# Performance work log

Hardware: AMD Instinct MI355X
Metric: run time of the kernel (lower is better)

Reference implementation:

```python
import jax, jax.numpy as jnp
import numpy as np

B = 32; N_NODES = 1000; WINDOW = 4; D = 128; N_PARTS = 10
T = 2; T_INT = 1; T_TEMP = 1
N_TOTAL = B * WINDOW * N_NODES
E_INT = 200000; E_TEMP = 96000


def setup_inputs() -> dict:
    key = jax.random.key(0)
    ks = jax.random.split(key, 24)
    inp = {}
    inp["node_inputs"] = jax.random.randint(ks[0], (B, N_NODES), 0, 10)
    inp["node_indices"] = jax.random.randint(ks[1], (E_INT,), 0, N_TOTAL)
    inp["neighbour_indices"] = jax.random.randint(ks[2], (E_INT,), 0, N_TOTAL)
    inp["temp_node_indices"] = jax.random.randint(ks[3], (E_TEMP,), 0, N_TOTAL)
    inp["temp_neighbour_indices"] = jax.random.randint(ks[4], (E_TEMP,), 0, N_TOTAL)

    def dense(k, din, dout):
        return jax.random.normal(k, (din, dout), jnp.float32) * np.float32(1.0 / np.sqrt(din))

    inp["embed_table"] = jax.random.normal(ks[5], (10, D), jnp.float32)
    # message MLP: 2*D -> 64 -> 64 -> 64 -> 64 -> D (4 gelu hidden, linear out)
    inp["msg_W_in"] = dense(ks[6], 2 * D, 64); inp["msg_b_in"] = jnp.zeros((64,), jnp.float32)
    inp["msg_W_hid"] = jax.random.normal(ks[7], (3, 64, 64), jnp.float32) * np.float32(1.0 / 8.0)
    inp["msg_b_hid"] = jnp.zeros((3, 64), jnp.float32)
    inp["msg_W_out"] = dense(ks[8], 64, D); inp["msg_b_out"] = jnp.zeros((D,), jnp.float32)
    # readout MLP: D -> 64 -> 64 -> 64 -> 64 -> n_parts
    inp["ro_W_in"] = dense(ks[9], D, 64); inp["ro_b_in"] = jnp.zeros((64,), jnp.float32)
    inp["ro_W_hid"] = jax.random.normal(ks[10], (3, 64, 64), jnp.float32) * np.float32(1.0 / 8.0)
    inp["ro_b_hid"] = jnp.zeros((3, 64), jnp.float32)
    inp["ro_W_out"] = dense(ks[11], 64, N_PARTS); inp["ro_b_out"] = jnp.zeros((N_PARTS,), jnp.float32)
    # GRU cells (tf.keras reset_after=True): kernel [D,3D], recurrent [D,3D], input+recurrent biases
    for nm, base in (("gi", 12), ("gt", 16)):
        inp[nm + "_Wx"] = dense(ks[base], D, 3 * D)
        inp[nm + "_Wh"] = dense(ks[base + 1], D, 3 * D)
        inp[nm + "_bi"] = jnp.zeros((3 * D,), jnp.float32)
        inp[nm + "_br"] = jnp.zeros((3 * D,), jnp.float32)
    return inp


def _mlp(x, W_in, b_in, W_hid, b_hid, W_out, b_out):
    h = jax.nn.gelu(x @ W_in + b_in, approximate=False)
    for i in range(W_hid.shape[0]):
        h = jax.nn.gelu(h @ W_hid[i] + b_hid[i], approximate=False)
    return h @ W_out + b_out


def _gru(h, x, Wx, Wh, bi, br):
    # tf.keras GRUCell, reset_after=True
    xz, xr, xh = jnp.split(x @ Wx + bi, 3, axis=1)
    hz, hr, hh = jnp.split(h @ Wh + br, 3, axis=1)
    z = jax.nn.sigmoid(xz + hz)
    r = jax.nn.sigmoid(xr + hr)
    cand = jnp.tanh(xh + r * hh)
    return z * h + (1.0 - z) * cand


def _message_mean(h, ni, bi, msg_p):
    g0 = h[ni]              # [E, D] node gather
    g1 = h[bi]              # [E, D] neighbour gather
    x = jnp.concatenate([jnp.concatenate([g0, g1], 1), jnp.concatenate([g1, g0], 1)], 0)  # [2E, 2D]
    msg = _mlp(x, *msg_p)   # [2E, D]
    seg = jnp.concatenate([bi, ni], 0)
    s = jax.ops.segment_sum(msg, seg, num_segments=h.shape[0])
    c = jax.ops.segment_sum(jnp.ones((seg.shape[0], 1), msg.dtype), seg, num_segments=h.shape[0])
    return s / jnp.maximum(c, 1.0)


def reference(node_inputs, node_indices, neighbour_indices, temp_node_indices, temp_neighbour_indices,
              embed_table, msg_W_in, msg_b_in, msg_W_hid, msg_b_hid, msg_W_out, msg_b_out,
              ro_W_in, ro_b_in, ro_W_hid, ro_b_hid, ro_W_out, ro_b_out,
              gi_Wx, gi_Wh, gi_bi, gi_br, gt_Wx, gt_Wh, gt_bi, gt_br):
    msg_p = (msg_W_in, msg_b_in, msg_W_hid, msg_b_hid, msg_W_out, msg_b_out)
    h = embed_table[node_inputs]                       # [B, N, D]
    h = jnp.repeat(h, WINDOW, axis=0).reshape(-1, D)   # [B*W*N, D]
    for _ in range(T):
        for _ in range(T_INT):
            m = _message_mean(h, node_indices, neighbour_indices, msg_p)
            h = _gru(h, m, gi_Wx, gi_Wh, gi_bi, gi_br)
        for _ in range(T_TEMP):
            m = _message_mean(h, temp_node_indices, temp_neighbour_indices, msg_p)
            h = _gru(h, m, gt_Wx, gt_Wh, gt_bi, gt_br)
    ridx = jnp.arange(N_NODES)[None, :] + jnp.arange(B)[:, None] * (WINDOW * N_NODES)
    return _mlp(h[ridx], ro_W_in, ro_b_in, ro_W_hid, ro_b_hid, ro_W_out, ro_b_out)  # [B, N, n_parts]
```

## Files before the change

### kernel.cpp

```cpp
#include <hip/hip_runtime.h>
#include <math.h>


#define DDIM 128
#define NTOT 128000
#define HBYTES 65536000ULL
#define EBLK 128

typedef unsigned short u16;
using f32x4 = __attribute__((ext_vector_type(4))) float;
using s16x8 = __attribute__((ext_vector_type(8))) short;

__device__ __forceinline__ float fast_rcp(float x) {
    return __builtin_amdgcn_rcpf(x);
}
__device__ __forceinline__ float gelu_exact(float x) {
    return 0.5f * x * (1.0f + erff(x * 0.70710678118654752440f));
}
__device__ __forceinline__ float gelu_fast(float x) {
    const float ax = fabsf(x) * 0.70710678118654752440f;
    const float t  = fast_rcp(1.0f + 0.3275911f * ax);
    const float poly = t * (0.254829592f + t * (-0.284496736f +
                       t * (1.421413741f + t * (-1.453152027f +
                       t * 1.061405429f))));
    const float e = __expf(-ax * ax);
    const float erfax = 1.0f - poly * e;
    const float erfv = copysignf(erfax, x);
    return 0.5f * x * (1.0f + erfv);
}
__device__ __forceinline__ float sigmoid_fast(float x) {
    return fast_rcp(1.0f + __expf(-x));
}
__device__ __forceinline__ float tanh_fast(float x) {
    const float e = __expf(2.0f * x);
    return 1.0f - 2.0f * fast_rcp(e + 1.0f);
}
__device__ __forceinline__ u16 f2bf(float x) {
    unsigned u = __float_as_uint(x);
    u += 0x7fffu + ((u >> 16) & 1u);
    return (u16)(u >> 16);
}
__device__ __forceinline__ float bf2f(u16 h) {
    return __uint_as_float(((unsigned)h) << 16);
}

__global__ __launch_bounds__(256) void embed_kernel(
    const int* __restrict__ inp, const float* __restrict__ table,
    float* __restrict__ h)
{
    int gid = blockIdx.x * 256 + threadIdx.x;
    if (gid >= NTOT * 32) return;
    int row = gid >> 5;
    int q   = gid & 31;
    int b   = row / 4000;
    int n   = (row % 4000) % 1000;
    int e   = inp[b * 1000 + n];
    ((float4*)h)[gid] = ((const float4*)table)[e * 32 + q];
}

__global__ __launch_bounds__(256) void hist_kernel(
    const int* __restrict__ ni, const int* __restrict__ bi, int E,
    int* __restrict__ deg)
{
    int g = blockIdx.x * 256 + threadIdx.x;
    if (g < E)          atomicAdd(&deg[bi[g]], 1);
    else if (g < 2 * E) atomicAdd(&deg[ni[g - E]], 1);
}

__global__ __launch_bounds__(256) void blockscan_kernel(
    const int* __restrict__ deg, int* __restrict__ offp, int* __restrict__ bsum)
{
    __shared__ int s[256];
    int tid = threadIdx.x;
    int i = blockIdx.x * 256 + tid;
    int v = deg[i];
    s[tid] = v;
    __syncthreads();
    for (int off = 1; off < 256; off <<= 1) {
        int t = (tid >= off) ? s[tid - off] : 0;
        __syncthreads();
        s[tid] += t;
        __syncthreads();
    }
    offp[i] = s[tid] - v;
    if (tid == 255) bsum[blockIdx.x] = s[255];
}

__global__ __launch_bounds__(512) void bscan_kernel(
    const int* __restrict__ bsum, int* __restrict__ bexc, int nb)
{
    __shared__ int s[512];
    int t = threadIdx.x;
    int v = (t < nb) ? bsum[t] : 0;
    s[t] = v;
    __syncthreads();
    for (int off = 1; off < 512; off <<= 1) {
        int u = (t >= off) ? s[t - off] : 0;
        __syncthreads();
        s[t] += u;
        __syncthreads();
    }
    if (t < nb) bexc[t] = s[t] - v;
}

__global__ __launch_bounds__(256) void fill_kernel(
    const int* __restrict__ ni, const int* __restrict__ bi, int E,
    const int* __restrict__ offp, const int* __restrict__ bexc,
    int* __restrict__ cursor, int* __restrict__ elist, int* __restrict__ slotseg)
{
    int g = blockIdx.x * 256 + threadIdx.x;
    if (g >= 2 * E) return;
    int seg = (g < E) ? bi[g] : ni[g - E];
    int pos = atomicAdd(&cursor[seg], 1);
    int slot = offp[seg] + bexc[seg >> 8] + pos;
    elist[slot] = g;
    slotseg[slot] = seg;
}

__global__ __launch_bounds__(256) void straddle_kernel(
    const int* __restrict__ slotseg, int nblocks32,
    int* __restrict__ list, int* __restrict__ count)
{
    int b = blockIdx.x * 256 + threadIdx.x + 1;
    if (b >= nblocks32) return;
    int s = slotseg[b * 32];
    if (s >= 0 && slotseg[b * 32 - 1] == s) {
        int pos = atomicAdd(count, 1);
        list[pos] = s;
    }
}

__global__ __launch_bounds__(64) void zero_rows_kernel(
    const int* __restrict__ list, const int* __restrict__ count,
    float* __restrict__ sbuf)
{
    int i = blockIdx.x;
    if (i >= *count) return;
    int seg = list[i];
    float4* row = (float4*)(sbuf + (size_t)seg * 64);
    if (threadIdx.x < 16) row[threadIdx.x] = make_float4(0.f, 0.f, 0.f, 0.f);
}

__global__ __launch_bounds__(256) void pack_gateB_kernel(
    const float* __restrict__ Wx, const float* __restrict__ Wh,
    u16* __restrict__ BH, u16* __restrict__ BL)
{
    int idx = blockIdx.x * 256 + threadIdx.x;
    if (idx >= 131072) return;
    int j    = idx & 7;
    int lane = (idx >> 3) & 63;
    int ntG  = (idx >> 9) & 31;
    int ktG  = idx >> 14;
    int k = ktG * 32 + (lane >> 4) * 8 + j;
    int n = ntG * 16 + (lane & 15);
    int g = n >> 7, jj = n & 127;
    float v;
    if (g == 0)      v = (k < 128) ? Wx[k * 384 + jj]       : Wh[(k - 128) * 384 + jj];
    else if (g == 1) v = (k < 128) ? Wx[k * 384 + 128 + jj] : Wh[(k - 128) * 384 + 128 + jj];
    else if (g == 2) v = (k < 128) ? Wx[k * 384 + 256 + jj] : 0.0f;
    else             v = (k < 128) ? 0.0f                   : Wh[(k - 128) * 384 + 256 + jj];
    u16 hb = f2bf(v);
    BH[idx] = hb;
    BL[idx] = f2bf(v - bf2f(hb));
}

__global__ __launch_bounds__(256) void pack_preB_kernel(
    const float* __restrict__ Win, u16* __restrict__ BH, u16* __restrict__ BL)
{
    int idx = blockIdx.x * 256 + threadIdx.x;
    if (idx >= 16384) return;
    int j    = idx & 7;
    int lane = (idx >> 3) & 63;
    int nt2  = (idx >> 9) & 7;
    int kt2  = idx >> 12;
    int k = kt2 * 32 + (lane >> 4) * 8 + j;
    int n = nt2 * 16 + (lane & 15);
    float v = (n < 64) ? Win[k * 64 + n] : Win[(128 + k) * 64 + (n - 64)];
    u16 hb = f2bf(v);
    BH[idx] = hb;
    BL[idx] = f2bf(v - bf2f(hb));
}

__global__ __launch_bounds__(256) void pack_hidB_kernel(
    const float* __restrict__ Whid, u16* __restrict__ BH, u16* __restrict__ BL)
{
    int idx = blockIdx.x * 256 + threadIdx.x;
    if (idx >= 12288) return;
    int j    = idx & 7;
    int lane = (idx >> 3) & 63;
    int nt   = (idx >> 9) & 3;
    int kt   = (idx >> 11) & 1;
    int L    = idx >> 12;
    int k = kt * 32 + (lane >> 4) * 8 + j;
    int n = nt * 16 + (lane & 15);
    float v = Whid[L * 4096 + k * 64 + n];
    u16 hb = f2bf(v);
    BH[idx] = hb;
    BL[idx] = f2bf(v - bf2f(hb));
}

__global__ __launch_bounds__(256) void pack_outB_kernel(
    const float* __restrict__ Wout, u16* __restrict__ BH, u16* __restrict__ BL)
{
    int idx = blockIdx.x * 256 + threadIdx.x;
    if (idx >= 8192) return;
    int j    = idx & 7;
    int lane = (idx >> 3) & 63;
    int nt   = (idx >> 9) & 7;
    int kt   = idx >> 12;
    int k = kt * 32 + (lane >> 4) * 8 + j;
    int n = nt * 16 + (lane & 15);
    float v = Wout[k * 128 + n];
    u16 hb = f2bf(v);
    BH[idx] = hb;
    BL[idx] = f2bf(v - bf2f(hb));
}

__global__ __launch_bounds__(256) void node_pre_kernel(
    const float* __restrict__ h, const float* __restrict__ Win,
    const float* __restrict__ bin, float* __restrict__ p)
{
    const int node = blockIdx.x * 256 + threadIdx.x;
    const float4* h4 = (const float4*)(h + (size_t)node * DDIM);
    float* prow = p + (size_t)node * DDIM;

    for (int c = 0; c < 4; ++c) {
        const int top   = (c < 2) ? 1 : 0;
        const int j0    = (c & 1) * 32;
        const int kbase = top ? 0 : 128;
        float acc[32];
        #pragma unroll
        for (int j = 0; j < 32; ++j) acc[j] = top ? bin[j0 + j] : 0.0f;
        for (int k4 = 0; k4 < 32; ++k4) {
            float4 hv = h4[k4];
            #pragma unroll
            for (int kk = 0; kk < 4; ++kk) {
                const float hk = (&hv.x)[kk];
                const float* wr = Win + (size_t)(kbase + k4 * 4 + kk) * 64 + j0;
                #pragma unroll
                for (int j = 0; j < 32; ++j) acc[j] = fmaf(hk, wr[j], acc[j]);
            }
        }
        float* dst = prow + (top ? 0 : 64) + j0;
        #pragma unroll
        for (int q = 0; q < 8; ++q)
            ((float4*)dst)[q] = make_float4(acc[q*4], acc[q*4+1],
                                            acc[q*4+2], acc[q*4+3]);
    }
}

__global__ __launch_bounds__(512) void edge_mlp_mfma(
    const int* __restrict__ ni, const int* __restrict__ bi, int E,
    const int* __restrict__ elist, const int* __restrict__ slotseg,
    const float* __restrict__ p,
    const u16* __restrict__ BhH, const u16* __restrict__ BhL,
    const float* __restrict__ bhid,
    float* __restrict__ sbuf)
{
    __shared__ short smA[17408];
    __shared__ int   segLDS[EBLK];
    __shared__ int   segedge[2];
    float* scat = (float*)smA;

    const int tid  = threadIdx.x;
    const int lane = tid & 63;
    const int w    = tid >> 6;
    const int s0   = blockIdx.x * EBLK;

    if (tid < 128) segLDS[tid] = slotseg[s0 + tid];
    if (tid == 0) segedge[0] = slotseg[s0 - 1];
    if (tid == 1) segedge[1] = slotseg[s0 + EBLK];

    {
        const int m  = (tid & 15) | (w << 4);
        const int gg = (tid >> 4) & 3;
        const int slot = s0 + m;
        const int g = elist[slot];
        int first, second;
        if (g < E) { first = ni[g];     second = bi[g];     }
        else       { first = bi[g - E]; second = ni[g - E]; }
        #pragma unroll
        for (int kt = 0; kt < 2; ++kt) {
            const int k0 = kt * 32 + gg * 8;
            const float4* pa = (const float4*)(p + (size_t)first  * DDIM + k0);
            const float4* pb = (const float4*)(p + (size_t)second * DDIM + 64 + k0);
            const float4 a0 = pa[0], a1 = pa[1], b0 = pb[0], b1 = pb[1];
            float x[8] = { a0.x + b0.x, a0.y + b0.y, a0.z + b0.z, a0.w + b0.w,
                           a1.x + b1.x, a1.y + b1.y, a1.z + b1.z, a1.w + b1.w };
            s16x8 hi8, lo8;
            #pragma unroll
            for (int j = 0; j < 8; ++j) {
                const float v = gelu_fast(x[j]);
                u16 hb = f2bf(v);
                hi8[j] = (short)hb;
                lo8[j] = (short)f2bf(v - bf2f(hb));
            }
            const int off = (kt * 8 + w) * 512 + lane * 8;
            *(s16x8*)(smA + off)        = hi8;
            *(s16x8*)(smA + 8192 + off) = lo8;
        }
    }

    const int mt = w;
    for (int L = 0; L < 2; ++L) {
        f32x4 acc[4];
        #pragma unroll
        for (int nt = 0; nt < 4; ++nt) {
            const float bv = bhid[L * 64 + nt * 16 + (lane & 15)];
            acc[nt] = (f32x4){bv, bv, bv, bv};
        }
        #pragma unroll
        for (int kt = 0; kt < 2; ++kt) {
            const s16x8 aH = *(const s16x8*)(smA + (kt * 8 + mt) * 512 + lane * 8);
            const s16x8 aL = *(const s16x8*)(smA + 8192 + (kt * 8 + mt) * 512 + lane * 8);
            #pragma unroll
            for (int nt = 0; nt < 4; ++nt) {
                const int bidx = (L * 8 + kt * 4 + nt) * 64 + lane;
                const s16x8 bH = ((const s16x8*)BhH)[bidx];
                const s16x8 bL = ((const s16x8*)BhL)[bidx];
                acc[nt] = __builtin_amdgcn_mfma_f32_16x16x32_bf16(aH, bH, acc[nt], 0, 0, 0);
                acc[nt] = __builtin_amdgcn_mfma_f32_16x16x32_bf16(aH, bL, acc[nt], 0, 0, 0);
                acc[nt] = __builtin_amdgcn_mfma_f32_16x16x32_bf16(aL, bH, acc[nt], 0, 0, 0);
            }
        }
        #pragma unroll
        for (int nt = 0; nt < 4; ++nt) {
            #pragma unroll
            for (int r = 0; r < 4; ++r) {
                const float v = gelu_fast(acc[nt][r]);
                const int ml  = (lane >> 4) * 4 + r;
                const int k   = nt * 16 + (lane & 15);
                const int kt2 = k >> 5, gg = (k >> 3) & 3, j = k & 7;
                const int off = (kt2 * 8 + mt) * 512 + (ml + 16 * gg) * 8 + j;
                u16 hb = f2bf(v);
                smA[off]        = (short)hb;
                smA[8192 + off] = (short)f2bf(v - bf2f(hb));
            }
        }
    }

    float gl[4][4];
    {
        f32x4 acc[4];
        #pragma unroll
        for (int nt = 0; nt < 4; ++nt) {
            const float bv = bhid[2 * 64 + nt * 16 + (lane & 15)];
            acc[nt] = (f32x4){bv, bv, bv, bv};
        }
        #pragma unroll
        for (int kt = 0; kt < 2; ++kt) {
            const s16x8 aH = *(const s16x8*)(smA + (kt * 8 + mt) * 512 + lane * 8);
            const s16x8 aL = *(const s16x8*)(smA + 8192 + (kt * 8 + mt) * 512 + lane * 8);
            #pragma unroll
            for (int nt = 0; nt < 4; ++nt) {
                const int bidx = (2 * 8 + kt * 4 + nt) * 64 + lane;
                const s16x8 bH = ((const s16x8*)BhH)[bidx];
                const s16x8 bL = ((const s16x8*)BhL)[bidx];
                acc[nt] = __builtin_amdgcn_mfma_f32_16x16x32_bf16(aH, bH, acc[nt], 0, 0, 0);
                acc[nt] = __builtin_amdgcn_mfma_f32_16x16x32_bf16(aH, bL, acc[nt], 0, 0, 0);
                acc[nt] = __builtin_amdgcn_mfma_f32_16x16x32_bf16(aL, bH, acc[nt], 0, 0, 0);
            }
        }
        #pragma unroll
        for (int nt = 0; nt < 4; ++nt)
            #pragma unroll
            for (int r = 0; r < 4; ++r)
                gl[nt][r] = gelu_fast(acc[nt][r]);
    }

    __syncthreads();
    #pragma unroll
    for (int nt = 0; nt < 4; ++nt)
        #pragma unroll
        for (int r = 0; r < 4; ++r)
            scat[(mt * 16 + (lane >> 4) * 4 + r) * 68 + nt * 16 + (lane & 15)]
                = gl[nt][r];
    __syncthreads();

    if (tid < 256) {
        const int col = tid & 63;
        const int r0  = (tid >> 6) * 32;
        const int r1  = r0 + 32;
        int   runSeg = -2;
        float runacc = 0.0f;
        bool  leftC  = true;
        for (int rowi = r0; rowi < r1; ++rowi) {
            const int sg = segLDS[rowi];
            const float v = scat[rowi * 68 + col];
            if (sg != runSeg) {
                if (runSeg >= 0) {
                    float* pp = sbuf + (size_t)runSeg * 64 + col;
                    if (leftC) *pp = runacc;
                    else       atomicAdd(pp, runacc);
                }
                runSeg = sg;
                runacc = v;
                if (rowi == r0) {
                    const int prev = (rowi == 0) ? segedge[0] : segLDS[rowi - 1];
                    leftC = (prev != sg);
                } else {
                    leftC = true;
                }
            } else {
                runacc += v;
            }
        }
        if (runSeg >= 0) {
            const int nxt = (r1 == 128) ? segedge[1] : segLDS[r1];
            const bool rightC = (nxt != runSeg);
            float* pp = sbuf + (size_t)runSeg * 64 + col;
            if (leftC && rightC) *pp = runacc;
            else                 atomicAdd(pp, runacc);
        }
    }
}

__global__ __launch_bounds__(256, 3) void gru_mfma_kernel(
    float* __restrict__ hio, const float* __restrict__ Ssum,
    const int* __restrict__ deg,
    const u16* __restrict__ WoH, const u16* __restrict__ WoL,
    const float* __restrict__ bo,
    const u16* __restrict__ BgH, const u16* __restrict__ BgL,
    const float* __restrict__ bi_, const float* __restrict__ br_,
    const u16* __restrict__ BpH, const u16* __restrict__ BpL,
    const float* __restrict__ binp,
    float* __restrict__ pout)
{
    __shared__ short sm[16384];
    __shared__ float ci_s[64];
    const int tid  = threadIdx.x;
    const int lane = tid & 63;
    const int w    = tid >> 6;
    const int jg   = w & 1;
    const int mh   = w >> 1;
    const int nbase = blockIdx.x * 64;

    const int mS = tid >> 2, q = tid & 3;
    const int nodeS = nbase + mS;
    const int laneS = (mS & 15) + 16 * q;
    const int seg_m = mS >> 4;
    const int dg = deg[nodeS];
    const float ci = (dg > 0) ? fast_rcp((float)dg) : 0.0f;
    ci_s[mS] = ci;

    #pragma unroll
    for (int c = 0; c < 2; ++c) {
        const int kl = c * 32 + q * 8;
        const float* src = Ssum + (size_t)nodeS * 64 + kl;
        const float4 v0 = ((const float4*)src)[0];
        const float4 v1 = ((const float4*)src)[1];
        float xv[8] = { v0.x * ci, v0.y * ci, v0.z * ci, v0.w * ci,
                        v1.x * ci, v1.y * ci, v1.z * ci, v1.w * ci };
        s16x8 hi8, lo8;
        #pragma unroll
        for (int i = 0; i < 8; ++i) {
            u16 hb = f2bf(xv[i]);
            hi8[i] = (short)hb;
            lo8[i] = (short)f2bf(xv[i] - bf2f(hb));
        }
        const int off = (c * 4 + seg_m) * 512 + laneS * 8;
        *(s16x8*)(sm + off)        = hi8;
        *(s16x8*)(sm + off + 8192) = lo8;
    }
    __syncthreads();

    f32x4 am[2][4];
    #pragma unroll
    for (int mf = 0; mf < 2; ++mf)
        #pragma unroll
        for (int t4 = 0; t4 < 4; ++t4)
            am[mf][t4] = (f32x4){0.f, 0.f, 0.f, 0.f};
    {
        const s16x8* WH8 = (const s16x8*)WoH;
        const s16x8* WL8 = (const s16x8*)WoL;
        #pragma unroll
        for (int kt = 0; kt < 2; ++kt) {
            const int a0off = (kt * 4 + 2 * mh) * 512 + lane * 8;
            const s16x8 aH0 = *(const s16x8*)(sm + a0off);
            const s16x8 aL0 = *(const s16x8*)(sm + 8192 + a0off);
            const s16x8 aH1 = *(const s16x8*)(sm + a0off + 512);
            const s16x8 aL1 = *(const s16x8*)(sm + 8192 + a0off + 512);
            #pragma unroll
            for (int t4 = 0; t4 < 4; ++t4) {
                const int idx = (kt * 8 + jg * 4 + t4) * 64 + lane;
                const s16x8 bH = WH8[idx];
                const s16x8 bL = WL8[idx];
                am[0][t4] = __builtin_amdgcn_mfma_f32_16x16x32_bf16(aH0, bH, am[0][t4], 0, 0, 0);
                am[0][t4] = __builtin_amdgcn_mfma_f32_16x16x32_bf16(aH0, bL, am[0][t4], 0, 0, 0);
                am[0][t4] = __builtin_amdgcn_mfma_f32_16x16x32_bf16(aL0, bH, am[0][t4], 0, 0, 0);
                am[1][t4] = __builtin_amdgcn_mfma_f32_16x16x32_bf16(aH1, bH, am[1][t4], 0, 0, 0);
                am[1][t4] = __builtin_amdgcn_mfma_f32_16x16x32_bf16(aH1, bL, am[1][t4], 0, 0, 0);
                am[1][t4] = __builtin_amdgcn_mfma_f32_16x16x32_bf16(aL1, bH, am[1][t4], 0, 0, 0);
            }
        }
    }
    __syncthreads();

    #pragma unroll
    for (int t4 = 0; t4 < 4; ++t4) {
        const int n = jg * 64 + t4 * 16 + (lane & 15);
        const float bv = bo[n];
        const int kt2 = n >> 5, gg = (n >> 3) & 3, jj = n & 7;
        #pragma unroll
        for (int mf = 0; mf < 2; ++mf) {
            const int mtile = 2 * mh + mf;
            #pragma unroll
            for (int r = 0; r < 4; ++r) {
                const int m15 = (lane >> 4) * 4 + r;
                const float cin = ci_s[mtile * 16 + m15];
                const float mv = am[mf][t4][r] + ((cin > 0.0f) ? bv : 0.0f);
                const int off = (kt2 * 4 + mtile) * 512 + (m15 + 16 * gg) * 8 + jj;
                u16 hb = f2bf(mv);
                sm[off]        = (short)hb;
                sm[off + 8192] = (short)f2bf(mv - bf2f(hb));
            }
        }
    }
    __syncthreads();

    f32x4 acc[2][4][4];
    #pragma unroll
    for (int mf = 0; mf < 2; ++mf)
        #pragma unroll
        for (int g = 0; g < 4; ++g)
            #pragma unroll
            for (int t4 = 0; t4 < 4; ++t4)
                acc[mf][g][t4] = (f32x4){0.f, 0.f, 0.f, 0.f};

    const s16x8* Bh8 = (const s16x8*)BgH;
    const s16x8* Bl8 = (const s16x8*)BgL;
    #pragma unroll
    for (int kt = 0; kt < 4; ++kt) {
        const int a0off = (kt * 4 + 2 * mh) * 512 + lane * 8;
        const s16x8 aH0 = *(const s16x8*)(sm + a0off);
        const s16x8 aL0 = *(const s16x8*)(sm + 8192 + a0off);
        const s16x8 aH1 = *(const s16x8*)(sm + a0off + 512);
        const s16x8 aL1 = *(const s16x8*)(sm + 8192 + a0off + 512);
        #pragma unroll
        for (int g = 0; g < 3; ++g) {
            #pragma unroll
            for (int t4 = 0; t4 < 4; ++t4) {
                const int idx = (kt * 32 + g * 8 + jg * 4 + t4) * 64 + lane;
                const s16x8 bH = Bh8[idx];
                const s16x8 bL = Bl8[idx];
                acc[0][g][t4] = __builtin_amdgcn_mfma_f32_16x16x32_bf16(aH0, bH, acc[0][g][t4], 0, 0, 0);
                acc[0][g][t4] = __builtin_amdgcn_mfma_f32_16x16x32_bf16(aH0, bL, acc[0][g][t4], 0, 0, 0);
                acc[0][g][t4] = __builtin_amdgcn_mfma_f32_16x16x32_bf16(aL0, bH, acc[0][g][t4], 0, 0, 0);
                acc[1][g][t4] = __builtin_amdgcn_mfma_f32_16x16x32_bf16(aH1, bH, acc[1][g][t4], 0, 0, 0);
                acc[1][g][t4] = __builtin_amdgcn_mfma_f32_16x16x32_bf16(aH1, bL, acc[1][g][t4], 0, 0, 0);
                acc[1][g][t4] = __builtin_amdgcn_mfma_f32_16x16x32_bf16(aL1, bH, acc[1][g][t4], 0, 0, 0);
            }
        }
    }
    __syncthreads();

    #pragma unroll
    for (int c = 0; c < 4; ++c) {
        const int kl = c * 32 + q * 8;
        const float* src = hio + (size_t)nodeS * DDIM + kl;
        const float4 v0 = ((const float4*)src)[0];
        const float4 v1 = ((const float4*)src)[1];
        float xv[8] = { v0.x, v0.y, v0.z, v0.w, v1.x, v1.y, v1.z, v1.w };
        s16x8 hi8, lo8;
        #pragma unroll
        for (int i = 0; i < 8; ++i) {
            u16 hb = f2bf(xv[i]);
            hi8[i] = (short)hb;
            lo8[i] = (short)f2bf(xv[i] - bf2f(hb));
        }
        const int off = (c * 4 + seg_m) * 512 + laneS * 8;
        *(s16x8*)(sm + off)        = hi8;
        *(s16x8*)(sm + off + 8192) = lo8;
    }
    __syncthreads();

    #pragma unroll
    for (int kt = 0; kt < 4; ++kt) {
        const int ktG = 4 + kt;
        const int a0off = (kt * 4 + 2 * mh) * 512 + lane * 8;
        const s16x8 aH0 = *(const s16x8*)(sm + a0off);
        const s16x8 aL0 = *(const s16x8*)(sm + 8192 + a0off);
        const s16x8 aH1 = *(const s16x8*)(sm + a0off + 512);
        const s16x8 aL1 = *(const s16x8*)(sm + 8192 + a0off + 512);
        #pragma unroll
        for (int gi = 0; gi < 3; ++gi) {
            const int g = (gi == 2) ? 3 : gi;
            #pragma unroll
            for (int t4 = 0; t4 < 4; ++t4) {
                const int idx = (ktG * 32 + g * 8 + jg * 4 + t4) * 64 + lane;
                const s16x8 bH = Bh8[idx];
                const s16x8 bL = Bl8[idx];
                acc[0][g][t4] = __builtin_amdgcn_mfma_f32_16x16x32_bf16(aH0, bH, acc[0][g][t4], 0, 0, 0);
                acc[0][g][t4] = __builtin_amdgcn_mfma_f32_16x16x32_bf16(aH0, bL, acc[0][g][t4], 0, 0, 0);
                acc[0][g][t4] = __builtin_amdgcn_mfma_f32_16x16x32_bf16(aL0, bH, acc[0][g][t4], 0, 0, 0);
                acc[1][g][t4] = __builtin_amdgcn_mfma_f32_16x16x32_bf16(aH1, bH, acc[1][g][t4], 0, 0, 0);
                acc[1][g][t4] = __builtin_amdgcn_mfma_f32_16x16x32_bf16(aH1, bL, acc[1][g][t4], 0, 0, 0);
                acc[1][g][t4] = __builtin_amdgcn_mfma_f32_16x16x32_bf16(aL1, bH, acc[1][g][t4], 0, 0, 0);
            }
        }
    }

    float hn[2][4][4];
    #pragma unroll
    for (int t4 = 0; t4 < 4; ++t4) {
        const int j = jg * 64 + t4 * 16 + (lane & 15);
        const float b_az = bi_[j]       + br_[j];
        const float b_ar = bi_[128 + j] + br_[128 + j];
        const float b_xh = bi_[256 + j];
        const float b_hh = br_[256 + j];
        const int jbase = (j >> 5) * 2048 + ((j >> 3) & 3) * 128 + (j & 7);
        #pragma unroll
        for (int mf = 0; mf < 2; ++mf) {
            const int mtile = 2 * mh + mf;
            #pragma unroll
            for (int r = 0; r < 4; ++r) {
                const int m15 = (lane >> 4) * 4 + r;
                const int off = jbase + mtile * 512 + m15 * 8;
                const float hv = bf2f((u16)sm[off]) + bf2f((u16)sm[8192 + off]);
                const int m = mtile * 16 + m15;
                const float az = acc[mf][0][t4][r] + b_az;
                const float ar = acc[mf][1][t4][r] + b_ar;
                const float xh = acc[mf][2][t4][r] + b_xh;
                const float hh = acc[mf][3][t4][r] + b_hh;
                const float z    = sigmoid_fast(az);
                const float rr   = sigmoid_fast(ar);
                const float cand = tanh_fast(xh + rr * hh);
                const float v    = z * hv + (1.0f - z) * cand;
                hio[(size_t)(nbase + m) * DDIM + j] = v;
                hn[mf][t4][r] = v;
            }
        }
    }
    __syncthreads();

    #pragma unroll
    for (int mf = 0; mf < 2; ++mf) {
        const int mtile = 2 * mh + mf;
        #pragma unroll
        for (int t4 = 0; t4 < 4; ++t4) {
            #pragma unroll
            for (int r = 0; r < 4; ++r) {
                const int m15 = (lane >> 4) * 4 + r;
                const int j   = jg * 64 + t4 * 16 + (lane & 15);
                const int kt2 = j >> 5, gg = (j >> 3) & 3, jj = j & 7;
                const int off = (kt2 * 4 + mtile) * 512 + (m15 + 16 * gg) * 8 + jj;
                const float v = hn[mf][t4][r];
                u16 hb = f2bf(v);
                sm[off]        = (short)hb;
                sm[off + 8192] = (short)f2bf(v - bf2f(hb));
            }
        }
    }
    __syncthreads();

    f32x4 acc2[2][4];
    #pragma unroll
    for (int mf = 0; mf < 2; ++mf)
        #pragma unroll
        for (int t4 = 0; t4 < 4; ++t4)
            acc2[mf][t4] = (f32x4){0.f, 0.f, 0.f, 0.f};

    const s16x8* Ph8 = (const s16x8*)BpH;
    const s16x8* Pl8 = (const s16x8*)BpL;
    #pragma unroll
    for (int kt2 = 0; kt2 < 4; ++kt2) {
        const int a0off = (kt2 * 4 + 2 * mh) * 512 + lane * 8;
        const s16x8 aH0 = *(const s16x8*)(sm + a0off);
        const s16x8 aL0 = *(const s16x8*)(sm + 8192 + a0off);
        const s16x8 aH1 = *(const s16x8*)(sm + a0off + 512);
        const s16x8 aL1 = *(const s16x8*)(sm + 8192 + a0off + 512);
        #pragma unroll
        for (int t4 = 0; t4 < 4; ++t4) {
            const int idx = (kt2 * 8 + jg * 4 + t4) * 64 + lane;
            const s16x8 bH = Ph8[idx];
            const s16x8 bL = Pl8[idx];
            acc2[0][t4] = __builtin_amdgcn_mfma_f32_16x16x32_bf16(aH0, bH, acc2[0][t4], 0, 0, 0);
            acc2[0][t4] = __builtin_amdgcn_mfma_f32_16x16x32_bf16(aH0, bL, acc2[0][t4], 0, 0, 0);
            acc2[0][t4] = __builtin_amdgcn_mfma_f32_16x16x32_bf16(aL0, bH, acc2[0][t4], 0, 0, 0);
            acc2[1][t4] = __builtin_amdgcn_mfma_f32_16x16x32_bf16(aH1, bH, acc2[1][t4], 0, 0, 0);
            acc2[1][t4] = __builtin_amdgcn_mfma_f32_16x16x32_bf16(aH1, bL, acc2[1][t4], 0, 0, 0);
            acc2[1][t4] = __builtin_amdgcn_mfma_f32_16x16x32_bf16(aL1, bH, acc2[1][t4], 0, 0, 0);
        }
    }
    #pragma unroll
    for (int mf = 0; mf < 2; ++mf) {
        const int mtile = 2 * mh + mf;
        #pragma unroll
        for (int t4 = 0; t4 < 4; ++t4) {
            const int n = jg * 64 + t4 * 16 + (lane & 15);
            const float badd = (n < 64) ? binp[n] : 0.0f;
            #pragma unroll
            for (int r = 0; r < 4; ++r) {
                const int m = mtile * 16 + (lane >> 4) * 4 + r;
                pout[(size_t)(nbase + m) * DDIM + n] = acc2[mf][t4][r] + badd;
            }
        }
    }
}

__global__ __launch_bounds__(64) void readout_kernel(
    const float* __restrict__ h,
    const float* __restrict__ Win,  const float* __restrict__ bin,
    const float* __restrict__ Whid, const float* __restrict__ bhid,
    const float* __restrict__ Wout, const float* __restrict__ bout,
    float* __restrict__ out)
{
    __shared__ float xs[64 * 65];
    const int tid = threadIdx.x;
    const int row = blockIdx.x * 64 + tid;
    const int b = row / 1000, n = row % 1000;
    const float4* xrow = (const float4*)(h + ((size_t)b * 4000 + n) * DDIM);

    {
        float acc[64];
        #pragma unroll
        for (int j = 0; j < 64; ++j) acc[j] = bin[j];
        #pragma unroll 2
        for (int k4 = 0; k4 < 32; ++k4) {
            float4 xv = xrow[k4];
            #pragma unroll
            for (int kk = 0; kk < 4; ++kk) {
                const float xk = (&xv.x)[kk];
                const float* wr = Win + (size_t)(k4 * 4 + kk) * 64;
                #pragma unroll
                for (int j = 0; j < 64; ++j) acc[j] = fmaf(xk, wr[j], acc[j]);
            }
        }
        #pragma unroll
        for (int j = 0; j < 64; ++j) xs[tid * 65 + j] = gelu_exact(acc[j]);
    }

    for (int L = 0; L < 3; ++L) {
        float acc[64];
        #pragma unroll
        for (int j = 0; j < 64; ++j) acc[j] = bhid[L * 64 + j];
        #pragma unroll 4
        for (int k = 0; k < 64; ++k) {
            const float xk = xs[tid * 65 + k];
            const float* wr = Whid + (size_t)L * 4096 + (size_t)k * 64;
            #pragma unroll
            for (int j = 0; j < 64; ++j) acc[j] = fmaf(xk, wr[j], acc[j]);
        }
        #pragma unroll
        for (int j = 0; j < 64; ++j) xs[tid * 65 + j] = gelu_exact(acc[j]);
    }

    float acc[10];
    #pragma unroll
    for (int pj = 0; pj < 10; ++pj) acc[pj] = bout[pj];
    #pragma unroll 4
    for (int k = 0; k < 64; ++k) {
        const float xk = xs[tid * 65 + k];
        const float* wr = Wout + k * 10;
        #pragma unroll
        for (int pj = 0; pj < 10; ++pj) acc[pj] = fmaf(xk, wr[pj], acc[pj]);
    }
    #pragma unroll
    for (int pj = 0; pj < 10; ++pj) out[(size_t)row * 10 + pj] = acc[pj];
}

extern "C" void kernel_launch(void* const* d_in, const int* in_sizes, int n_in,
                              void* d_out, int out_size, void* d_ws, size_t ws_size,
                              hipStream_t stream) {
    const int*   node_inputs = (const int*)d_in[0];
    const int*   ni_int = (const int*)d_in[1];
    const int*   bi_int = (const int*)d_in[2];
    const int*   ni_tmp = (const int*)d_in[3];
    const int*   bi_tmp = (const int*)d_in[4];
    const float* embed  = (const float*)d_in[5];
    const float* mWin   = (const float*)d_in[6];
    const float* mbin   = (const float*)d_in[7];
    const float* mWhid  = (const float*)d_in[8];
    const float* mbhid  = (const float*)d_in[9];
    const float* mWout  = (const float*)d_in[10];
    const float* mbout  = (const float*)d_in[11];
    const float* roWin  = (const float*)d_in[12];
    const float* robin  = (const float*)d_in[13];
    const float* roWhid = (const float*)d_in[14];
    const float* robhid = (const float*)d_in[15];
    const float* roWout = (const float*)d_in[16];
    const float* robout = (const float*)d_in[17];
    const float* giWx = (const float*)d_in[18];
    const float* giWh = (const float*)d_in[19];
    const float* gibi = (const float*)d_in[20];
    const float* gibr = (const float*)d_in[21];
    const float* gtWx = (const float*)d_in[22];
    const float* gtWh = (const float*)d_in[23];
    const float* gtbi = (const float*)d_in[24];
    const float* gtbr = (const float*)d_in[25];
    float* out = (float*)d_out;

    const int E_INT = 200000, E_TMP = 96000;
    const int NSLOT_I = 400000;
    const int NSLOT_T = 192000;
    const int NBLK_I = NSLOT_I / EBLK;
    const int NBLK_T = NSLOT_T / EBLK;
    const int NS32_I = NSLOT_I / 32;
    const int NS32_T = NSLOT_T / 32;

    char* ws = (char*)d_ws;
    float* B0 = (float*)(ws);
    float* B1 = (float*)(ws + HBYTES);
    float* B2 = (float*)(ws + 2 * HBYTES);
    char*  ib = ws + 3 * HBYTES;

    int* deg_i   = (int*)(ib);
    int* deg_t   = (int*)(ib + 512000);
    int* offp_i  = (int*)(ib + 1024000);
    int* offp_t  = (int*)(ib + 1536000);
    int* bexc_i  = (int*)(ib + 2048000);
    int* bexc_t  = (int*)(ib + 2052096);
    int* bsum    = (int*)(ib + 2056192);
    int* cursor  = (int*)(ib + 2060288);
    int* el_i    = (int*)(ib + 2572288);
    int* el_t    = (int*)(ib + 4172288);
    int* ssi_raw = (int*)(ib + 4940288);
    int* sst_raw = (int*)(ib + 6540296);
    char* fb = ib + 8114176;
    u16* BgiH = (u16*)(fb);
    u16* BgiL = (u16*)(fb +  262144);
    u16* BgtH = (u16*)(fb +  524288);
    u16* BgtL = (u16*)(fb +  786432);
    u16* BpH  = (u16*)(fb + 1048576);
    u16* BpL  = (u16*)(fb + 1081344);
    u16* EhH  = (u16*)(fb + 1114112);
    u16* EhL  = (u16*)(fb + 1138688);
    u16* EoH  = (u16*)(fb + 1163264);
    u16* EoL  = (u16*)(fb + 1179648);
    int* str_i  = (int*)(fb + 1196032);
    int* str_t  = (int*)(fb + 1246032);
    int* strc_i = (int*)(fb + 1270032);
    int* strc_t = (int*)(fb + 1270036);
    int* ssi = ssi_raw + 1;
    int* sst = sst_raw + 1;

    embed_kernel<<<16000, 256, 0, stream>>>(node_inputs, embed, B0);

    hipMemsetAsync(deg_i, 0, NTOT * sizeof(int), stream);
    hipMemsetAsync(deg_t, 0, NTOT * sizeof(int), stream);
    hist_kernel<<<(2 * E_INT + 255) / 256, 256, 0, stream>>>(ni_int, bi_int, E_INT, deg_i);
    hist_kernel<<<(2 * E_TMP + 255) / 256, 256, 0, stream>>>(ni_tmp, bi_tmp, E_TMP, deg_t);

    hipMemsetAsync(ssi_raw, 0xFF, (size_t)(NSLOT_I + 2) * sizeof(int), stream);
    hipMemsetAsync(sst_raw, 0xFF, (size_t)(NSLOT_T + 2) * sizeof(int), stream);

    blockscan_kernel<<<500, 256, 0, stream>>>(deg_i, offp_i, bsum);
    bscan_kernel<<<1, 512, 0, stream>>>(bsum, bexc_i, 500);
    hipMemsetAsync(cursor, 0, NTOT * sizeof(int), stream);
    fill_kernel<<<(2 * E_INT + 255) / 256, 256, 0, stream>>>(
        ni_int, bi_int, E_INT, offp_i, bexc_i, cursor, el_i, ssi);

    blockscan_kernel<<<500, 256, 0, stream>>>(deg_t, offp_t, bsum);
    bscan_kernel<<<1, 512, 0, stream>>>(bsum, bexc_t, 500);
    hipMemsetAsync(cursor, 0, NTOT * sizeof(int), stream);
    fill_kernel<<<(2 * E_TMP + 255) / 256, 256, 0, stream>>>(
        ni_tmp, bi_tmp, E_TMP, offp_t, bexc_t, cursor, el_t, sst);

    hipMemsetAsync(strc_i, 0, sizeof(int), stream);
    hipMemsetAsync(strc_t, 0, sizeof(int), stream);
    straddle_kernel<<<(NS32_I + 255) / 256, 256, 0, stream>>>(ssi, NS32_I, str_i, strc_i);
    straddle_kernel<<<(NS32_T + 255) / 256, 256, 0, stream>>>(sst, NS32_T, str_t, strc_t);

    pack_gateB_kernel<<<512, 256, 0, stream>>>(giWx, giWh, BgiH, BgiL);
    pack_gateB_kernel<<<512, 256, 0, stream>>>(gtWx, gtWh, BgtH, BgtL);
    pack_preB_kernel<<<64, 256, 0, stream>>>(mWin, BpH, BpL);
    pack_hidB_kernel<<<48, 256, 0, stream>>>(mWhid, EhH, EhL);
    pack_outB_kernel<<<32, 256, 0, stream>>>(mWout, EoH, EoL);

    node_pre_kernel<<<NTOT / 256, 256, 0, stream>>>(B0, mWin, mbin, B1);

    for (int ph = 0; ph < 4; ++ph) {
        const bool isInt = (ph % 2 == 0);
        if (isInt) {
            zero_rows_kernel<<<NS32_I, 64, 0, stream>>>(str_i, strc_i, B2);
            edge_mlp_mfma<<<NBLK_I, 512, 0, stream>>>(
                ni_int, bi_int, E_INT, el_i, ssi, B1,
                EhH, EhL, mbhid, B2);
            gru_mfma_kernel<<<NTOT / 64, 256, 0, stream>>>(
                B0, B2, deg_i, EoH, EoL, mbout,
                BgiH, BgiL, gibi, gibr, BpH, BpL, mbin, B1);
        } else {
            zero_rows_kernel<<<NS32_T, 64, 0, stream>>>(str_t, strc_t, B2);
            edge_mlp_mfma<<<NBLK_T, 512, 0, stream>>>(
                ni_tmp, bi_tmp, E_TMP, el_t, sst, B1,
                EhH, EhL, mbhid, B2);
            gru_mfma_kernel<<<NTOT / 64, 256, 0, stream>>>(
                B0, B2, deg_t, EoH, EoL, mbout,
                BgtH, BgtL, gtbi, gtbr, BpH, BpL, mbin, B1);
        }
    }

    readout_kernel<<<500, 64, 0, stream>>>(
        B0, roWin, robin, roWhid, robhid, roWout, robout, out);
}
```

Baseline: 1.456 ms.

## Move node pre-projection to MFMA and double GRU block size to 128 nodes

Replaces the scalar-FMA node_pre kernel with an MFMA version that splits h into bf16 hi/lo parts in LDS and reuses the packed pre-projection weights. The GRU kernel grows from 64 to 128 nodes per block with 512 threads, and its LDS layout strides are doubled. The ci_s shared array is replaced by reloading degree flags per lane. The node_pre change targets a compute-bound one-off projection. The larger GRU blocks are meant to amortise weight fetches, at the cost of more LDS per block and lower occupancy.

New measurement: 1.603 ms. +10.1%, slower.

```diff
diff --git a/kernel.cpp b/kernel.cpp
--- a/kernel.cpp
+++ b/kernel.cpp
@@ -216,36 +216,86 @@
     BL[idx] = f2bf(v - bf2f(hb));
 }
 
-__global__ __launch_bounds__(256) void node_pre_kernel(
-    const float* __restrict__ h, const float* __restrict__ Win,
-    const float* __restrict__ bin, float* __restrict__ p)
-{
-    const int node = blockIdx.x * 256 + threadIdx.x;
-    const float4* h4 = (const float4*)(h + (size_t)node * DDIM);
-    float* prow = p + (size_t)node * DDIM;
-
+__global__ __launch_bounds__(512, 2) void node_pre_mfma(
+    const float* __restrict__ h,
+    const u16* __restrict__ BpH, const u16* __restrict__ BpL,
+    const float* __restrict__ binp, float* __restrict__ pout)
+{
+    __shared__ short sm[32768];
+    const int tid  = threadIdx.x;
+    const int lane = tid & 63;
+    const int w    = tid >> 6;
+    const int jg   = w & 1;
+    const int mh   = w >> 1;
+    const int nbase = blockIdx.x * 128;
+
+    const int mS = tid >> 2, q = tid & 3;
+    const int nodeS = nbase + mS;
+    const int laneS = (mS & 15) + 16 * q;
+    const int seg_m = mS >> 4;
+
+    #pragma unroll
     for (int c = 0; c < 4; ++c) {
-        const int top   = (c < 2) ? 1 : 0;
-        const int j0    = (c & 1) * 32;
-        const int kbase = top ? 0 : 128;
-        float acc[32];
-        #pragma unroll
-        for (int j = 0; j < 32; ++j) acc[j] = top ? bin[j0 + j] : 0.0f;
-        for (int k4 = 0; k4 < 32; ++k4) {
-            float4 hv = h4[k4];
-            #pragma unroll
-            for (int kk = 0; kk < 4; ++kk) {
-                const float hk = (&hv.x)[kk];
-                const float* wr = Win + (size_t)(kbase + k4 * 4 + kk) * 64 + j0;
-                #pragma unroll
-                for (int j = 0; j < 32; ++j) acc[j] = fmaf(hk, wr[j], acc[j]);
-            }
-        }
-        float* dst = prow + (top ? 0 : 64) + j0;
-        #pragma unroll
-        for (int q = 0; q < 8; ++q)
-            ((float4*)dst)[q] = make_float4(acc[q*4], acc[q*4+1],
-                                            acc[q*4+2], acc[q*4+3]);
+        const int kl = c * 32 + q * 8;
+        const float* src = h + (size_t)nodeS * DDIM + kl;
+        const float4 v0 = ((const float4*)src)[0];
+        const float4 v1 = ((const float4*)src)[1];
+        float xv[8] = { v0.x, v0.y, v0.z, v0.w, v1.x, v1.y, v1.z, v1.w };
+        s16x8 hi8, lo8;
+        #pragma unroll
+        for (int i = 0; i < 8; ++i) {
+            u16 hb = f2bf(xv[i]);
+            hi8[i] = (short)hb;
+            lo8[i] = (short)f2bf(xv[i] - bf2f(hb));
+        }
+        const int off = (c * 8 + seg_m) * 512 + laneS * 8;
+        *(s16x8*)(sm + off)         = hi8;
+        *(s16x8*)(sm + off + 16384) = lo8;
+    }
+    __syncthreads();
+
+    f32x4 acc2[2][4];
+    #pragma unroll
+    for (int mf = 0; mf < 2; ++mf)
+        #pragma unroll
+        for (int t4 = 0; t4 < 4; ++t4)
+            acc2[mf][t4] = (f32x4){0.f, 0.f, 0.f, 0.f};
+
+    const s16x8* Ph8 = (const s16x8*)BpH;
+    const s16x8* Pl8 = (const s16x8*)BpL;
+    #pragma unroll
+    for (int kt2 = 0; kt2 < 4; ++kt2) {
+        const int a0off = (kt2 * 8 + 2 * mh) * 512 + lane * 8;
+        const s16x8 aH0 = *(const s16x8*)(sm + a0off);
+        const s16x8 aL0 = *(const s16x8*)(sm + 16384 + a0off);
+        const s16x8 aH1 = *(const s16x8*)(sm + a0off + 512);
+        const s16x8 aL1 = *(const s16x8*)(sm + 16384 + a0off + 512);
+        #pragma unroll
+        for (int t4 = 0; t4 < 4; ++t4) {
+            const int idx = (kt2 * 8 + jg * 4 + t4) * 64 + lane;
+            const s16x8 bH = Ph8[idx];
+            const s16x8 bL = Pl8[idx];
+            acc2[0][t4] = __builtin_amdgcn_mfma_f32_16x16x32_bf16(aH0, bH, acc2[0][t4], 0, 0, 0);
+            acc2[0][t4] = __builtin_amdgcn_mfma_f32_16x16x32_bf16(aH0, bL, acc2[0][t4], 0, 0, 0);
+            acc2[0][t4] = __builtin_amdgcn_mfma_f32_16x16x32_bf16(aL0, bH, acc2[0][t4], 0, 0, 0);
+            acc2[1][t4] = __builtin_amdgcn_mfma_f32_16x16x32_bf16(aH1, bH, acc2[1][t4], 0, 0, 0);
+            acc2[1][t4] = __builtin_amdgcn_mfma_f32_16x16x32_bf16(aH1, bL, acc2[1][t4], 0, 0, 0);
+            acc2[1][t4] = __builtin_amdgcn_mfma_f32_16x16x32_bf16(aL1, bH, acc2[1][t4], 0, 0, 0);
+        }
+    }
+    #pragma unroll
+    for (int mf = 0; mf < 2; ++mf) {
+        const int mtile = 2 * mh + mf;
+        #pragma unroll
+        for (int t4 = 0; t4 < 4; ++t4) {
+            const int n = jg * 64 + t4 * 16 + (lane & 15);
+            const float badd = (n < 64) ? binp[n] : 0.0f;
+            #pragma unroll
+            for (int r = 0; r < 4; ++r) {
+                const int m = mtile * 16 + (lane >> 4) * 4 + r;
+                pout[(size_t)(nbase + m) * DDIM + n] = acc2[mf][t4][r] + badd;
+            }
+        }
     }
 }
 
@@ -415,7 +465,7 @@
     }
 }
 
-__global__ __launch_bounds__(256, 3) void gru_mfma_kernel(
+__global__ __launch_bounds__(512, 2) void gru_mfma_kernel(
     float* __restrict__ hio, const float* __restrict__ Ssum,
     const int* __restrict__ deg,
     const u16* __restrict__ WoH, const u16* __restrict__ WoL,
@@ -426,14 +476,13 @@
     const float* __restrict__ binp,
     float* __restrict__ pout)
 {
-    __shared__ short sm[16384];
-    __shared__ float ci_s[64];
+    __shared__ short sm[32768];
     const int tid  = threadIdx.x;
     const int lane = tid & 63;
     const int w    = tid >> 6;
     const int jg   = w & 1;
     const int mh   = w >> 1;
-    const int nbase = blockIdx.x * 64;
+    const int nbase = blockIdx.x * 128;
 
     const int mS = tid >> 2, q = tid & 3;
     const int nodeS = nbase + mS;
@@ -441,7 +490,6 @@
     const int seg_m = mS >> 4;
     const int dg = deg[nodeS];
     const float ci = (dg > 0) ? fast_rcp((float)dg) : 0.0f;
-    ci_s[mS] = ci;
 
     #pragma unroll
     for (int c = 0; c < 2; ++c) {
@@ -458,9 +506,9 @@
             hi8[i] = (short)hb;
             lo8[i] = (short)f2bf(xv[i] - bf2f(hb));
         }
-        const int off = (c * 4 + seg_m) * 512 + laneS * 8;
-        *(s16x8*)(sm + off)        = hi8;
-        *(s16x8*)(sm + off + 8192) = lo8;
+        const int off = (c * 8 + seg_m) * 512 + laneS * 8;
+        *(s16x8*)(sm + off)         = hi8;
+        *(s16x8*)(sm + off + 16384) = lo8;
     }
     __syncthreads();
 
@@ -475,11 +523,11 @@
         const s16x8* WL8 = (const s16x8*)WoL;
         #pragma unroll
         for (int kt = 0; kt < 2; ++kt) {
-            const int a0off = (kt * 4 + 2 * mh) * 512 + lane * 8;
+            const int a0off = (kt * 8 + 2 * mh) * 512 + lane * 8;
             const s16x8 aH0 = *(const s16x8*)(sm + a0off);
-            const s16x8 aL0 = *(const s16x8*)(sm + 8192 + a0off);
+            const s16x8 aL0 = *(const s16x8*)(sm + 16384 + a0off);
             const s16x8 aH1 = *(const s16x8*)(sm + a0off + 512);
-            const s16x8 aL1 = *(const s16x8*)(sm + 8192 + a0off + 512);
+            const s16x8 aL1 = *(const s16x8*)(sm + 16384 + a0off + 512);
             #pragma unroll
             for (int t4 = 0; t4 < 4; ++t4) {
                 const int idx = (kt * 8 + jg * 4 + t4) * 64 + lane;
@@ -496,23 +544,30 @@
     }
     __syncthreads();
 
-    #pragma unroll
-    for (int t4 = 0; t4 < 4; ++t4) {
-        const int n = jg * 64 + t4 * 16 + (lane & 15);
-        const float bv = bo[n];
-        const int kt2 = n >> 5, gg = (n >> 3) & 3, jj = n & 7;
-        #pragma unroll
-        for (int mf = 0; mf < 2; ++mf) {
-            const int mtile = 2 * mh + mf;
-            #pragma unroll
-            for (int r = 0; r < 4; ++r) {
-                const int m15 = (lane >> 4) * 4 + r;
-                const float cin = ci_s[mtile * 16 + m15];
-                const float mv = am[mf][t4][r] + ((cin > 0.0f) ? bv : 0.0f);
-                const int off = (kt2 * 4 + mtile) * 512 + (m15 + 16 * gg) * 8 + jj;
-                u16 hb = f2bf(mv);
-                sm[off]        = (short)hb;
-                sm[off + 8192] = (short)f2bf(mv - bf2f(hb));
+    {
+        bool bon[2][4];
+        #pragma unroll
+        for (int mf = 0; mf < 2; ++mf)
+            #pragma unroll
+            for (int r = 0; r < 4; ++r)
+                bon[mf][r] = deg[nbase + (2 * mh + mf) * 16 + (lane >> 4) * 4 + r] > 0;
+        #pragma unroll
+        for (int t4 = 0; t4 < 4; ++t4) {
+            const int n = jg * 64 + t4 * 16 + (lane & 15);
+            const float bv = bo[n];
+            const int kt2 = n >> 5, gg = (n >> 3) & 3, jj = n & 7;
+            #pragma unroll
+            for (int mf = 0; mf < 2; ++mf) {
+                const int mtile = 2 * mh + mf;
+                #pragma unroll
+                for (int r = 0; r < 4; ++r) {
+                    const int m15 = (lane >> 4) * 4 + r;
+                    const float mv = am[mf][t4][r] + (bon[mf][r] ? bv : 0.0f);
+                    const int off = (kt2 * 8 + mtile) * 512 + (m15 + 16 * gg) * 8 + jj;
+                    u16 hb = f2bf(mv);
+                    sm[off]         = (short)hb;
+                    sm[off + 16384] = (short)f2bf(mv - bf2f(hb));
+                }
             }
         }
     }
@@ -531,11 +586,11 @@
     const s16x8* Bl8 = (const s16x8*)BgL;
     #pragma unroll
     for (int kt = 0; kt < 4; ++kt) {
-        const int a0off = (kt * 4 + 2 * mh) * 512 + lane * 8;
+        const int a0off = (kt * 8 + 2 * mh) * 512 + lane * 8;
         const s16x8 aH0 = *(const s16x8*)(sm + a0off);
-        const s16x8 aL0 = *(const s16x8*)(sm + 8192 + a0off);
+        const s16x8 aL0 = *(const s16x8*)(sm + 16384 + a0off);
         const s16x8 aH1 = *(const s16x8*)(sm + a0off + 512);
-        const s16x8 aL1 = *(const s16x8*)(sm + 8192 + a0off + 512);
+        const s16x8 aL1 = *(const s16x8*)(sm + 16384 + a0off + 512);
         #pragma unroll
         for (int g = 0; g < 3; ++g) {
             #pragma unroll
@@ -568,20 +623,20 @@
             hi8[i] = (short)hb;
             lo8[i] = (short)f2bf(xv[i] - bf2f(hb));
         }
-        const int off = (c * 4 + seg_m) * 512 + laneS * 8;
-        *(s16x8*)(sm + off)        = hi8;
-        *(s16x8*)(sm + off + 8192) = lo8;
+        const int off = (c * 8 + seg_m) * 512 + laneS * 8;
+        *(s16x8*)(sm + off)         = hi8;
+        *(s16x8*)(sm + off + 16384) = lo8;
     }
     __syncthreads();
 
     #pragma unroll
     for (int kt = 0; kt < 4; ++kt) {
         const int ktG = 4 + kt;
-        const int a0off = (kt * 4 + 2 * mh) * 512 + lane * 8;
+        const int a0off = (kt * 8 + 2 * mh) * 512 + lane * 8;
         const s16x8 aH0 = *(const s16x8*)(sm + a0off);
-        const s16x8 aL0 = *(const s16x8*)(sm + 8192 + a0off);
+        const s16x8 aL0 = *(const s16x8*)(sm + 16384 + a0off);
         const s16x8 aH1 = *(const s16x8*)(sm + a0off + 512);
-        const s16x8 aL1 = *(const s16x8*)(sm + 8192 + a0off + 512);
+        const s16x8 aL1 = *(const s16x8*)(sm + 16384 + a0off + 512);
         #pragma unroll
         for (int gi = 0; gi < 3; ++gi) {
             const int g = (gi == 2) ? 3 : gi;
@@ -608,7 +663,7 @@
         const float b_ar = bi_[128 + j] + br_[128 + j];
         const float b_xh = bi_[256 + j];
         const float b_hh = br_[256 + j];
-        const int jbase = (j >> 5) * 2048 + ((j >> 3) & 3) * 128 + (j & 7);
+        const int jbase = (j >> 5) * 4096 + ((j >> 3) & 3) * 128 + (j & 7);
         #pragma unroll
         for (int mf = 0; mf < 2; ++mf) {
             const int mtile = 2 * mh + mf;
@@ -616,7 +671,7 @@
             for (int r = 0; r < 4; ++r) {
                 const int m15 = (lane >> 4) * 4 + r;
                 const int off = jbase + mtile * 512 + m15 * 8;
-                const float hv = bf2f((u16)sm[off]) + bf2f((u16)sm[8192 + off]);
+                const float hv = bf2f((u16)sm[off]) + bf2f((u16)sm[16384 + off]);
                 const int m = mtile * 16 + m15;
                 const float az = acc[mf][0][t4][r] + b_az;
                 const float ar = acc[mf][1][t4][r] + b_ar;
@@ -643,11 +698,11 @@
                 const int m15 = (lane >> 4) * 4 + r;
                 const int j   = jg * 64 + t4 * 16 + (lane & 15);
                 const int kt2 = j >> 5, gg = (j >> 3) & 3, jj = j & 7;
-                const int off = (kt2 * 4 + mtile) * 512 + (m15 + 16 * gg) * 8 + jj;
+                const int off = (kt2 * 8 + mtile) * 512 + (m15 + 16 * gg) * 8 + jj;
                 const float v = hn[mf][t4][r];
                 u16 hb = f2bf(v);
-                sm[off]        = (short)hb;
-                sm[off + 8192] = (short)f2bf(v - bf2f(hb));
+                sm[off]         = (short)hb;
+                sm[off + 16384] = (short)f2bf(v - bf2f(hb));
             }
         }
     }
@@ -664,11 +719,11 @@
     const s16x8* Pl8 = (const s16x8*)BpL;
     #pragma unroll
     for (int kt2 = 0; kt2 < 4; ++kt2) {
-        const int a0off = (kt2 * 4 + 2 * mh) * 512 + lane * 8;
+        const int a0off = (kt2 * 8 + 2 * mh) * 512 + lane * 8;
         const s16x8 aH0 = *(const s16x8*)(sm + a0off);
-        const s16x8 aL0 = *(const s16x8*)(sm + 8192 + a0off);
+        const s16x8 aL0 = *(const s16x8*)(sm + 16384 + a0off);
         const s16x8 aH1 = *(const s16x8*)(sm + a0off + 512);
-        const s16x8 aL1 = *(const s16x8*)(sm + 8192 + a0off + 512);
+        const s16x8 aL1 = *(const s16x8*)(sm + 16384 + a0off + 512);
         #pragma unroll
         for (int t4 = 0; t4 < 4; ++t4) {
             const int idx = (kt2 * 8 + jg * 4 + t4) * 64 + lane;
@@ -867,7 +922,7 @@
     pack_hidB_kernel<<<48, 256, 0, stream>>>(mWhid, EhH, EhL);
     pack_outB_kernel<<<32, 256, 0, stream>>>(mWout, EoH, EoL);
 
-    node_pre_kernel<<<NTOT / 256, 256, 0, stream>>>(B0, mWin, mbin, B1);
+    node_pre_mfma<<<NTOT / 128, 512, 0, stream>>>(B0, BpH, BpL, mbin, B1);
 
     for (int ph = 0; ph < 4; ++ph) {
         const bool isInt = (ph % 2 == 0);
@@ -876,7 +931,7 @@
             edge_mlp_mfma<<<NBLK_I, 512, 0, stream>>>(
                 ni_int, bi_int, E_INT, el_i, ssi, B1,
                 EhH, EhL, mbhid, B2);
-            gru_mfma_kernel<<<NTOT / 64, 256, 0, stream>>>(
+            gru_mfma_kernel<<<NTOT / 128, 512, 0, stream>>>(
                 B0, B2, deg_i, EoH, EoL, mbout,
                 BgiH, BgiL, gibi, gibr, BpH, BpL, mbin, B1);
         } else {
@@ -884,7 +939,7 @@
             edge_mlp_mfma<<<NBLK_T, 512, 0, stream>>>(
                 ni_tmp, bi_tmp, E_TMP, el_t, sst, B1,
                 EhH, EhL, mbhid, B2);
-            gru_mfma_kernel<<<NTOT / 64, 256, 0, stream>>>(
+            gru_mfma_kernel<<<NTOT / 128, 512, 0, stream>>>(
                 B0, B2, deg_t, EoH, EoL, mbout,
                 BgtH, BgtL, gtbi, gtbr, BpH, BpL, mbin, B1);
         }
```
